# Optimization experiments

Measured on AMD Instinct MI355X. Metric: run time of the kernel, lower is better.

The kernel has to match this reference:

```python
import jax, jax.numpy as jnp
import numpy as np
import math

NEG = -1e9  # finite stand-in for -inf under masking (exactly zeroed by entmax support)

def entmax15(z):
    # Exact 1.5-entmax along last axis (Peters et al. 2019, sort-based).
    z = z / 2.0
    z = z - jnp.max(z, axis=-1, keepdims=True)            # shift-invariant
    zs = -jnp.sort(-z, axis=-1)                            # descending sort
    L = zs.shape[-1]
    k = jnp.arange(1, L + 1, dtype=z.dtype)
    mean = jnp.cumsum(zs, axis=-1) / k                     # running mean
    mean_sq = jnp.cumsum(zs * zs, axis=-1) / k             # running mean of squares
    ss = k * (mean_sq - mean * mean)
    delta = (1.0 - ss) / k
    tau = mean - jnp.sqrt(jnp.clip(delta, 0.0))
    support_size = jnp.sum(tau <= zs, axis=-1, keepdims=True)  # k*
    tau_star = jnp.take_along_axis(tau, support_size - 1, axis=-1)
    p = jnp.square(jnp.clip(z - tau_star, 0.0))
    return p

def setup_inputs() -> dict:
    key = jax.random.key(0)
    ks = jax.random.split(key, 7)
    B, L, D = 2, 1536, 768
    query = jax.random.normal(ks[0], (B, L, D), dtype=jnp.float32)
    kee = jax.random.normal(ks[1], (B, L, D), dtype=jnp.float32)
    mask = jax.random.randint(ks[2], (B, L), 0, 2, dtype=jnp.int32)
    s = 1.0 / math.sqrt(D)
    wq_w = jax.random.uniform(ks[3], (D, D), jnp.float32, -s, s)
    wq_b = jax.random.uniform(ks[4], (D,), jnp.float32, -s, s)
    wk_w = jax.random.uniform(ks[5], (D, D), jnp.float32, -s, s)
    wk_b = jax.random.uniform(ks[6], (D,), jnp.float32, -s, s)
    return {"query": query, "key": kee, "mask": mask,
            "wq_w": wq_w, "wq_b": wq_b, "wk_w": wk_w, "wk_b": wk_b}

def reference(query, key, mask, wq_w, wq_b, wk_w, wk_b):
    B, Lq, D = query.shape
    H = 12
    dk = D // H
    q = (query @ wq_w.T + wq_b).reshape(B, Lq, H, dk)
    k = (key @ wk_w.T + wk_b).reshape(B, -1, H, dk)
    # scores: [B, H, Lq, Lk]
    scores = jnp.einsum('bqhd,bkhd->bhqk', q, k) / math.sqrt(dk)
    kpm = (mask != 0)[:, None, None, :]                    # key padding mask
    scores = jnp.where(kpm, scores, NEG)
    p_attn = entmax15(scores)
    return jnp.sum(p_attn, axis=1) / H                     # [B, Lq, Lk]
```

## Files before the change

### kernel.cpp

```cpp
#include <hip/hip_runtime.h>
#include <math.h>

#define BB 2
#define LL 1536
#define DD 768
#define HH 12
#define DKK 64
#define ZNEG -5.0e8f

typedef __attribute__((ext_vector_type(8))) short bf16x8;
typedef __attribute__((ext_vector_type(8))) unsigned short u16x8;
typedef __attribute__((ext_vector_type(4))) float f32x4;

__device__ __forceinline__ unsigned short f32_to_bf16_rn(float x) {
    unsigned int u = __float_as_uint(x);
    u += 0x7fffu + ((u >> 16) & 1u);
    return (unsigned short)(u >> 16);
}
__device__ __forceinline__ float bf16u_to_f32(unsigned short h) {
    return __uint_as_float(((unsigned int)h) << 16);
}

__device__ __forceinline__ void split8(const float* __restrict__ gsrc,
                                       unsigned short* __restrict__ hdst,
                                       unsigned short* __restrict__ ldst) {
    float4 v0 = *reinterpret_cast<const float4*>(gsrc);
    float4 v1 = *reinterpret_cast<const float4*>(gsrc + 4);
    float f[8] = {v0.x, v0.y, v0.z, v0.w, v1.x, v1.y, v1.z, v1.w};
    u16x8 hi, lo;
    #pragma unroll
    for (int i = 0; i < 8; ++i) {
        unsigned short h = f32_to_bf16_rn(f[i]);
        float r = f[i] - bf16u_to_f32(h);
        hi[i] = h;
        lo[i] = f32_to_bf16_rn(r);
    }
    *reinterpret_cast<u16x8*>(hdst) = hi;
    *reinterpret_cast<u16x8*>(ldst) = lo;
}

__global__ __launch_bounds__(256) void proj_mfma(
    const float* __restrict__ Xq, const float* __restrict__ Xk,
    const float* __restrict__ Wq, const float* __restrict__ Wk,
    const float* __restrict__ bq, const float* __restrict__ bk,
    unsigned short* __restrict__ Qh, unsigned short* __restrict__ Ql,
    unsigned short* __restrict__ Kh, unsigned short* __restrict__ Kl)
{
    const float* X    = blockIdx.z ? Xk : Xq;
    const float* W    = blockIdx.z ? Wk : Wq;
    const float* bias = blockIdx.z ? bk : bq;
    unsigned short* Oh = blockIdx.z ? Kh : Qh;
    unsigned short* Ol = blockIdx.z ? Kl : Ql;

    __shared__ alignas(16) unsigned short Ah[8 * 64 * 8];
    __shared__ alignas(16) unsigned short Al[8 * 64 * 8];
    __shared__ alignas(16) unsigned short Bh[4 * 64 * 8];
    __shared__ alignas(16) unsigned short Bl[4 * 64 * 8];

    const int tid  = threadIdx.x;
    const int lane = tid & 63;
    const int w    = tid >> 6;
    const int wm   = w & 1;
    const int wn   = w >> 1;
    const int m0   = blockIdx.y * 128;
    const int n0   = blockIdx.x * 64;

    f32x4 acc[4][2] = {};

    for (int k0 = 0; k0 < DD; k0 += 32) {
        #pragma unroll
        for (int i = 0; i < 2; ++i) {
            const int c = tid + (i << 8);
            const int m = c >> 2, g = c & 3;
            const int slot = ((m >> 4) * 64 + (m & 15) + (g << 4)) * 8;
            split8(X + (size_t)(m0 + m) * DD + k0 + g * 8, Ah + slot, Al + slot);
        }
        {
            const int n = tid >> 2, g = tid & 3;
            const int slot = ((n >> 4) * 64 + (n & 15) + (g << 4)) * 8;
            split8(W + (size_t)(n0 + n) * DD + k0 + g * 8, Bh + slot, Bl + slot);
        }
        __syncthreads();

        bf16x8 aH[4], aL[4], bH[2], bL[2];
        #pragma unroll
        for (int fm = 0; fm < 4; ++fm) {
            const int f = wm * 4 + fm;
            aH[fm] = *reinterpret_cast<const bf16x8*>(Ah + (f * 64 + lane) * 8);
            aL[fm] = *reinterpret_cast<const bf16x8*>(Al + (f * 64 + lane) * 8);
        }
        #pragma unroll
        for (int fn = 0; fn < 2; ++fn) {
            const int f = wn * 2 + fn;
            bH[fn] = *reinterpret_cast<const bf16x8*>(Bh + (f * 64 + lane) * 8);
            bL[fn] = *reinterpret_cast<const bf16x8*>(Bl + (f * 64 + lane) * 8);
        }
        #pragma unroll
        for (int fm = 0; fm < 4; ++fm)
            #pragma unroll
            for (int fn = 0; fn < 2; ++fn) {
                acc[fm][fn] = __builtin_amdgcn_mfma_f32_16x16x32_bf16(aH[fm], bH[fn], acc[fm][fn], 0, 0, 0);
                acc[fm][fn] = __builtin_amdgcn_mfma_f32_16x16x32_bf16(aH[fm], bL[fn], acc[fm][fn], 0, 0, 0);
                acc[fm][fn] = __builtin_amdgcn_mfma_f32_16x16x32_bf16(aL[fm], bH[fn], acc[fm][fn], 0, 0, 0);
            }
        __syncthreads();
    }

    const int r0 = (lane >> 4) << 2;
    const int cl = lane & 15;
    #pragma unroll
    for (int fn = 0; fn < 2; ++fn) {
        const int col = n0 + wn * 32 + fn * 16 + cl;
        const float bv = bias[col];
        #pragma unroll
        for (int fm = 0; fm < 4; ++fm) {
            const int row = m0 + wm * 64 + fm * 16 + r0;
            #pragma unroll
            for (int r = 0; r < 4; ++r) {
                const float v = acc[fm][fn][r] + bv;
                const unsigned short h16 = f32_to_bf16_rn(v);
                const float res = v - bf16u_to_f32(h16);
                const size_t o = (size_t)(row + r) * DD + col;
                Oh[o] = h16;
                Ol[o] = f32_to_bf16_rn(res);
            }
        }
    }
}

__global__ __launch_bounds__(256) void scores_mfma(
    const unsigned short* __restrict__ Qh, const unsigned short* __restrict__ Ql,
    const unsigned short* __restrict__ Kh, const unsigned short* __restrict__ Kl,
    const int* __restrict__ mask, float* __restrict__ S)
{
    const int bh = blockIdx.z;
    const int b  = bh / HH;
    const int h  = bh - b * HH;
    const int q0 = blockIdx.y * 128;
    const int n0 = blockIdx.x * 64;

    __shared__ alignas(16) unsigned short Ah[8 * 2 * 64 * 8];
    __shared__ alignas(16) unsigned short Al[8 * 2 * 64 * 8];
    __shared__ alignas(16) unsigned short Bh[4 * 2 * 64 * 8];
    __shared__ alignas(16) unsigned short Bl[4 * 2 * 64 * 8];

    const int tid  = threadIdx.x;
    const int lane = tid & 63;
    const int w    = tid >> 6;
    const int wm   = w & 1;
    const int wn   = w >> 1;

    #pragma unroll
    for (int i = 0; i < 4; ++i) {
        const int c = tid + (i << 8);
        const int m = c >> 3, c8 = c & 7;
        const int qq = c8 >> 2, g = c8 & 3;
        const int slot = (((m >> 4) * 2 + qq) * 64 + (m & 15) + (g << 4)) * 8;
        const size_t o = (size_t)(b * LL + q0 + m) * DD + h * DKK + c8 * 8;
        *reinterpret_cast<u16x8*>(Ah + slot) = *reinterpret_cast<const u16x8*>(Qh + o);
        *reinterpret_cast<u16x8*>(Al + slot) = *reinterpret_cast<const u16x8*>(Ql + o);
    }
    #pragma unroll
    for (int i = 0; i < 2; ++i) {
        const int c = tid + (i << 8);
        const int n = c >> 3, c8 = c & 7;
        const int qq = c8 >> 2, g = c8 & 3;
        const int slot = (((n >> 4) * 2 + qq) * 64 + (n & 15) + (g << 4)) * 8;
        const size_t o = (size_t)(b * LL + n0 + n) * DD + h * DKK + c8 * 8;
        *reinterpret_cast<u16x8*>(Bh + slot) = *reinterpret_cast<const u16x8*>(Kh + o);
        *reinterpret_cast<u16x8*>(Bl + slot) = *reinterpret_cast<const u16x8*>(Kl + o);
    }
    __syncthreads();

    f32x4 acc[4][2] = {};
    #pragma unroll
    for (int qq = 0; qq < 2; ++qq) {
        bf16x8 aH[4], aL[4], bH[2], bL[2];
        #pragma unroll
        for (int fm = 0; fm < 4; ++fm) {
            const int f = (wm * 4 + fm) * 2 + qq;
            aH[fm] = *reinterpret_cast<const bf16x8*>(Ah + (f * 64 + lane) * 8);
            aL[fm] = *reinterpret_cast<const bf16x8*>(Al + (f * 64 + lane) * 8);
        }
        #pragma unroll
        for (int fn = 0; fn < 2; ++fn) {
            const int f = (wn * 2 + fn) * 2 + qq;
            bH[fn] = *reinterpret_cast<const bf16x8*>(Bh + (f * 64 + lane) * 8);
            bL[fn] = *reinterpret_cast<const bf16x8*>(Bl + (f * 64 + lane) * 8);
        }
        #pragma unroll
        for (int fm = 0; fm < 4; ++fm)
            #pragma unroll
            for (int fn = 0; fn < 2; ++fn) {
                acc[fm][fn] = __builtin_amdgcn_mfma_f32_16x16x32_bf16(aH[fm], bH[fn], acc[fm][fn], 0, 0, 0);
                acc[fm][fn] = __builtin_amdgcn_mfma_f32_16x16x32_bf16(aH[fm], bL[fn], acc[fm][fn], 0, 0, 0);
                acc[fm][fn] = __builtin_amdgcn_mfma_f32_16x16x32_bf16(aL[fm], bH[fn], acc[fm][fn], 0, 0, 0);
            }
    }

    const int r0 = (lane >> 4) << 2;
    const int cl = lane & 15;
    #pragma unroll
    for (int fn = 0; fn < 2; ++fn) {
        const int col = n0 + wn * 32 + fn * 16 + cl;
        const int mk  = mask[b * LL + col];
        #pragma unroll
        for (int fm = 0; fm < 4; ++fm) {
            const int row = q0 + wm * 64 + fm * 16 + r0;
            const size_t base = ((size_t)bh * LL + row) * LL + col;
            #pragma unroll
            for (int r = 0; r < 4; ++r) {
                const float v = acc[fm][fn][r] * 0.0625f;
                S[base + (size_t)r * LL] = mk ? v : ZNEG;
            }
        }
    }
}

__device__ __forceinline__ float waveReduceSum(float v) {
    #pragma unroll
    for (int off = 32; off > 0; off >>= 1) v += __shfl_xor(v, off, 64);
    return v;
}
__device__ __forceinline__ float waveReduceMax(float v) {
    #pragma unroll
    for (int off = 32; off > 0; off >>= 1) v = fmaxf(v, __shfl_xor(v, off, 64));
    return v;
}

__global__ __launch_bounds__(256) void entmax_sum(
    const float* __restrict__ S, float* __restrict__ out)
{
    const int bq = blockIdx.x;
    const int b  = bq / LL;
    const int q  = bq - b * LL;
    const int tid = threadIdx.x;
    const int w  = tid >> 6;
    const int l  = tid & 63;

    __shared__ float buf[4][LL];

    float acc[24];
    #pragma unroll
    for (int i = 0; i < 24; ++i) acc[i] = 0.0f;

    #pragma unroll
    for (int hh = 0; hh < 3; ++hh) {
        const int h = w + (hh << 2);
        const float* row = S + ((size_t)(b * HH + h) * LL + q) * LL + l * 24;

        float z[24];
        #pragma unroll
        for (int i = 0; i < 24; i += 4) {
            float4 v = *reinterpret_cast<const float4*>(row + i);
            z[i] = v.x; z[i + 1] = v.y; z[i + 2] = v.z; z[i + 3] = v.w;
        }

        float m = z[0];
        #pragma unroll
        for (int i = 1; i < 24; ++i) m = fmaxf(m, z[i]);
        m = waveReduceMax(m);
        #pragma unroll
        for (int i = 0; i < 24; ++i) z[i] -= m;

        float lo = -1.0f, hi_ = 0.0f;
        #pragma unroll
        for (int it = 0; it < 8; ++it) {
            const float tau = 0.5f * (lo + hi_);
            float s = 0.0f;
            #pragma unroll
            for (int i = 0; i < 24; ++i) {
                const float t = fmaxf(z[i] - tau, 0.0f);
                s = fmaf(t, t, s);
            }
            s = waveReduceSum(s);
            if (s >= 1.0f) lo = tau; else hi_ = tau;
        }

        float s1 = 0.0f, s2 = 0.0f, cn = 0.0f;
        #pragma unroll
        for (int i = 0; i < 24; ++i) {
            const bool a = z[i] > lo;
            const float t = a ? z[i] : 0.0f;
            s1 += t;
            s2 = fmaf(t, t, s2);
            cn += a ? 1.0f : 0.0f;
        }
        s1 = waveReduceSum(s1);
        s2 = waveReduceSum(s2);
        cn = waveReduceSum(cn);
        const float disc = fmaxf(fmaf(s1, s1, -cn * (s2 - 1.0f)), 0.0f);
        const float tau = (s1 - sqrtf(disc)) / cn;

        #pragma unroll
        for (int i = 0; i < 24; ++i) {
            const float t = fmaxf(z[i] - tau, 0.0f);
            acc[i] = fmaf(t, t, acc[i]);
        }
    }

    #pragma unroll
    for (int i = 0; i < 24; ++i) buf[w][l * 24 + i] = acc[i];
    __syncthreads();

    float* orow = out + (size_t)bq * LL;
    #pragma unroll
    for (int i = 0; i < 6; ++i) {
        const int c = tid + (i << 8);
        orow[c] = (buf[0][c] + buf[1][c] + buf[2][c] + buf[3][c]) * (1.0f / 12.0f);
    }
}

extern "C" void kernel_launch(void* const* d_in, const int* in_sizes, int n_in,
                              void* d_out, int out_size, void* d_ws, size_t ws_size,
                              hipStream_t stream) {
    (void)in_sizes; (void)n_in; (void)out_size; (void)ws_size;
    const float* query = (const float*)d_in[0];
    const float* key   = (const float*)d_in[1];
    const int*   mask  = (const int*)d_in[2];
    const float* wq_w  = (const float*)d_in[3];
    const float* wq_b  = (const float*)d_in[4];
    const float* wk_w  = (const float*)d_in[5];
    const float* wk_b  = (const float*)d_in[6];
    float* out = (float*)d_out;

    const size_t NE = (size_t)BB * LL * DD;
    unsigned short* Qh = (unsigned short*)d_ws;
    unsigned short* Ql = Qh + NE;
    unsigned short* Kh = Ql + NE;
    unsigned short* Kl = Kh + NE;
    float* S = (float*)(Kl + NE);

    proj_mfma<<<dim3(DD / 64, (BB * LL) / 128, 2), 256, 0, stream>>>(
        query, key, wq_w, wk_w, wq_b, wk_b, Qh, Ql, Kh, Kl);

    scores_mfma<<<dim3(LL / 64, LL / 128, BB * HH), 256, 0, stream>>>(
        Qh, Ql, Kh, Kl, mask, S);

    entmax_sum<<<BB * LL, 256, 0, stream>>>(S, out);
}
```

Measured before the change: 231.2 us.

## Pre-split inputs to bf16 hi/lo and load tiles via global_load_lds

```diff
diff --git a/kernel.cpp b/kernel.cpp
--- a/kernel.cpp
+++ b/kernel.cpp
@@ -39,15 +39,33 @@
     *reinterpret_cast<u16x8*>(ldst) = lo;
 }
 
+__device__ __forceinline__ void glds16(const unsigned short* g, unsigned short* s) {
+    __builtin_amdgcn_global_load_lds(
+        (const __attribute__((address_space(1))) unsigned short*)g,
+        (__attribute__((address_space(3))) unsigned short*)s, 16, 0, 0);
+}
+
+__global__ __launch_bounds__(256) void presplit(
+    const float* __restrict__ src,
+    unsigned short* __restrict__ h, unsigned short* __restrict__ l)
+{
+    const int i = (blockIdx.x * 256 + threadIdx.x) * 8;
+    split8(src + i, h + i, l + i);
+}
+
 __global__ __launch_bounds__(256) void proj_mfma(
-    const float* __restrict__ Xq, const float* __restrict__ Xk,
-    const float* __restrict__ Wq, const float* __restrict__ Wk,
+    const unsigned short* __restrict__ Xqh, const unsigned short* __restrict__ Xql,
+    const unsigned short* __restrict__ Xkh, const unsigned short* __restrict__ Xkl,
+    const unsigned short* __restrict__ Wqh, const unsigned short* __restrict__ Wql,
+    const unsigned short* __restrict__ Wkh, const unsigned short* __restrict__ Wkl,
     const float* __restrict__ bq, const float* __restrict__ bk,
     unsigned short* __restrict__ Qh, unsigned short* __restrict__ Ql,
     unsigned short* __restrict__ Kh, unsigned short* __restrict__ Kl)
 {
-    const float* X    = blockIdx.z ? Xk : Xq;
-    const float* W    = blockIdx.z ? Wk : Wq;
+    const unsigned short* Xh = blockIdx.z ? Xkh : Xqh;
+    const unsigned short* Xl = blockIdx.z ? Xkl : Xql;
+    const unsigned short* Wh = blockIdx.z ? Wkh : Wqh;
+    const unsigned short* Wl = blockIdx.z ? Wkl : Wql;
     const float* bias = blockIdx.z ? bk : bq;
     unsigned short* Oh = blockIdx.z ? Kh : Qh;
     unsigned short* Ol = blockIdx.z ? Kl : Ql;
@@ -65,21 +83,34 @@
     const int m0   = blockIdx.y * 128;
     const int n0   = blockIdx.x * 64;
 
+    int offA[2];
+    #pragma unroll
+    for (int j = 0; j < 2; ++j) {
+        const int s = w * 128 + j * 64 + lane;
+        const int m = ((s >> 6) << 4) | (s & 15);
+        const int g = (s >> 4) & 3;
+        offA[j] = (m0 + m) * DD + g * 8;
+    }
+    int offB;
+    {
+        const int s = w * 64 + lane;
+        const int n = ((s >> 6) << 4) | (s & 15);
+        const int g = (s >> 4) & 3;
+        offB = (n0 + n) * DD + g * 8;
+    }
+
     f32x4 acc[4][2] = {};
 
     for (int k0 = 0; k0 < DD; k0 += 32) {
         #pragma unroll
-        for (int i = 0; i < 2; ++i) {
-            const int c = tid + (i << 8);
-            const int m = c >> 2, g = c & 3;
-            const int slot = ((m >> 4) * 64 + (m & 15) + (g << 4)) * 8;
-            split8(X + (size_t)(m0 + m) * DD + k0 + g * 8, Ah + slot, Al + slot);
-        }
-        {
-            const int n = tid >> 2, g = tid & 3;
-            const int slot = ((n >> 4) * 64 + (n & 15) + (g << 4)) * 8;
-            split8(W + (size_t)(n0 + n) * DD + k0 + g * 8, Bh + slot, Bl + slot);
-        }
+        for (int j = 0; j < 2; ++j) {
+            unsigned short* dstH = Ah + (size_t)(w * 128 + j * 64) * 8;
+            unsigned short* dstL = Al + (size_t)(w * 128 + j * 64) * 8;
+            glds16(Xh + offA[j] + k0, dstH);
+            glds16(Xl + offA[j] + k0, dstL);
+        }
+        glds16(Wh + offB + k0, Bh + (size_t)(w * 64) * 8);
+        glds16(Wl + offB + k0, Bl + (size_t)(w * 64) * 8);
         __syncthreads();
 
         bf16x8 aH[4], aL[4], bH[2], bL[2];
@@ -151,24 +182,24 @@
     const int wn   = w >> 1;
 
     #pragma unroll
-    for (int i = 0; i < 4; ++i) {
-        const int c = tid + (i << 8);
-        const int m = c >> 3, c8 = c & 7;
-        const int qq = c8 >> 2, g = c8 & 3;
-        const int slot = (((m >> 4) * 2 + qq) * 64 + (m & 15) + (g << 4)) * 8;
-        const size_t o = (size_t)(b * LL + q0 + m) * DD + h * DKK + c8 * 8;
-        *reinterpret_cast<u16x8*>(Ah + slot) = *reinterpret_cast<const u16x8*>(Qh + o);
-        *reinterpret_cast<u16x8*>(Al + slot) = *reinterpret_cast<const u16x8*>(Ql + o);
-    }
-    #pragma unroll
-    for (int i = 0; i < 2; ++i) {
-        const int c = tid + (i << 8);
-        const int n = c >> 3, c8 = c & 7;
-        const int qq = c8 >> 2, g = c8 & 3;
-        const int slot = (((n >> 4) * 2 + qq) * 64 + (n & 15) + (g << 4)) * 8;
-        const size_t o = (size_t)(b * LL + n0 + n) * DD + h * DKK + c8 * 8;
-        *reinterpret_cast<u16x8*>(Bh + slot) = *reinterpret_cast<const u16x8*>(Kh + o);
-        *reinterpret_cast<u16x8*>(Bl + slot) = *reinterpret_cast<const u16x8*>(Kl + o);
+    for (int j = 0; j < 4; ++j) {
+        const int s = w * 256 + j * 64 + lane;
+        const int m  = ((s >> 7) << 4) | (s & 15);
+        const int qq = (s >> 6) & 1;
+        const int g  = (s >> 4) & 3;
+        const size_t o = (size_t)(b * LL + q0 + m) * DD + h * DKK + qq * 32 + g * 8;
+        glds16(Qh + o, Ah + (size_t)(w * 256 + j * 64) * 8);
+        glds16(Ql + o, Al + (size_t)(w * 256 + j * 64) * 8);
+    }
+    #pragma unroll
+    for (int j = 0; j < 2; ++j) {
+        const int s = w * 128 + j * 64 + lane;
+        const int n  = ((s >> 7) << 4) | (s & 15);
+        const int qq = (s >> 6) & 1;
+        const int g  = (s >> 4) & 3;
+        const size_t o = (size_t)(b * LL + n0 + n) * DD + h * DKK + qq * 32 + g * 8;
+        glds16(Kh + o, Bh + (size_t)(w * 128 + j * 64) * 8);
+        glds16(Kl + o, Bl + (size_t)(w * 128 + j * 64) * 8);
     }
     __syncthreads();
 
@@ -325,14 +356,29 @@
     float* out = (float*)d_out;
 
     const size_t NE = (size_t)BB * LL * DD;
+    const size_t NW = (size_t)DD * DD;
     unsigned short* Qh = (unsigned short*)d_ws;
     unsigned short* Ql = Qh + NE;
     unsigned short* Kh = Ql + NE;
     unsigned short* Kl = Kh + NE;
     float* S = (float*)(Kl + NE);
 
+    unsigned short* Xqh = (unsigned short*)S;
+    unsigned short* Xql = Xqh + NE;
+    unsigned short* Xkh = Xql + NE;
+    unsigned short* Xkl = Xkh + NE;
+    unsigned short* Wqh = Xkl + NE;
+    unsigned short* Wql = Wqh + NW;
+    unsigned short* Wkh = Wql + NW;
+    unsigned short* Wkl = Wkh + NW;
+
+    presplit<<<NE / 2048, 256, 0, stream>>>(query, Xqh, Xql);
+    presplit<<<NE / 2048, 256, 0, stream>>>(key,   Xkh, Xkl);
+    presplit<<<NW / 2048, 256, 0, stream>>>(wq_w,  Wqh, Wql);
+    presplit<<<NW / 2048, 256, 0, stream>>>(wk_w,  Wkh, Wkl);
+
     proj_mfma<<<dim3(DD / 64, (BB * LL) / 128, 2), 256, 0, stream>>>(
-        query, key, wq_w, wk_w, wq_b, wk_b, Qh, Ql, Kh, Kl);
+        Xqh, Xql, Xkh, Xkl, Wqh, Wql, Wkh, Wkl, wq_b, wk_b, Qh, Ql, Kh, Kl);
 
     scores_mfma<<<dim3(LL / 64, LL / 128, BB * HH), 256, 0, stream>>>(
         Qh, Ql, Kh, Kl, mask, S);
```

After: 260.1 us. +12.5%, slower.
